# Optimization experiments

Measured on AMD Instinct MI355X. Metric: run time of the kernel, lower is better.

The kernel has to match this reference:

```python
import jax, jax.numpy as jnp
import numpy as np

B, N, F_IN, F_OUT = 8, 2048, 128, 128


def setup_inputs() -> dict:
    key = jax.random.key(0)
    k1, k2, k3, k4 = jax.random.split(key, 4)
    h = jax.random.normal(k1, (B, N, F_IN), dtype=jnp.float32)
    adj = (jax.random.uniform(k2, (B, N, N)) > 0.5).astype(jnp.float32)
    adj = jnp.maximum(adj, jnp.eye(N, dtype=jnp.float32)[None])
    # torch nn.Linear weights: W is [out_features, in_features], a is [1, 2*out_features]
    W = jax.random.normal(k3, (F_OUT, F_IN), dtype=jnp.float32) * 0.05
    a = jax.random.normal(k4, (1, 2 * F_OUT), dtype=jnp.float32) * 0.05
    return {"h": h, "adj": adj, "W": W, "a": a}


def reference(h, adj, W, a):
    # Wh = W(h): [B, N, F_OUT]
    Wh = jnp.einsum("bnf,of->bno", h, W)
    # attn_fc(concat(Wh_i, Wh_j)) == (Wh_i @ a1) + (Wh_j @ a2): exact split of the
    # linear layer, avoiding the O(B*N*N*2F) concat intermediate.
    a1 = a[0, :F_OUT]
    a2 = a[0, F_OUT:]
    e_i = Wh @ a1  # [B, N]  score contribution of destination node i
    e_j = Wh @ a2  # [B, N]  score contribution of source node j
    e = e_i[:, :, None] + e_j[:, None, :]  # [B, N, N]
    e = e + (1.0 - adj) * (-1e9)
    alpha = jax.nn.softmax(e, axis=-1)  # [B, N, N]
    # weighted aggregation: h_out[b,i] = sum_j alpha[b,i,j] * Wh[b,j]
    h_out = jnp.einsum("bij,bjo->bio", alpha, Wh)
    return h_out
```

## Files before the change

kernel.cpp:

```cpp
#include <hip/hip_runtime.h>
#include <stdint.h>

#define AS1 __attribute__((address_space(1)))
#define AS3 __attribute__((address_space(3)))

typedef __bf16 bf16x8 __attribute__((ext_vector_type(8)));
typedef float f32x4 __attribute__((ext_vector_type(4)));

constexpr int NB = 8;
constexpr int N  = 2048;
constexpr int F  = 128;

__device__ __forceinline__ unsigned short bf16r(float f) {
    unsigned u = __float_as_uint(f);
    return (unsigned short)((u + 0x7FFFu + ((u >> 16) & 1u)) >> 16);
}
__device__ __forceinline__ float bf2f(unsigned short s) {
    return __uint_as_float(((unsigned)s) << 16);
}


__global__ __launch_bounds__(256) void k1_wh(const float* __restrict__ h,
                                             const float* __restrict__ W,
                                             const float* __restrict__ a,
                                             unsigned short* __restrict__ Wb2,
                                             unsigned short* __restrict__ p16) {
    __shared__ float epart[2][64];

    const int tid  = threadIdx.x;
    const int lane = tid & 63, wid = tid >> 6;
    const int quad = lane >> 4, l15 = lane & 15;
    const int wm = wid >> 1, wn = wid & 1;
    const int m0 = blockIdx.x * 64;
    const int batch = m0 >> 11;
    const int nbase = m0 & 2047;

    f32x4 acc[2][4] = {};

#pragma unroll
    for (int kk = 0; kk < 4; ++kk) {
        const int k = kk * 32 + quad * 8;
        bf16x8 afr[2], bfr[4];
#pragma unroll
        for (int rt = 0; rt < 2; ++rt) {
            const float* src = h + (size_t)(m0 + wm * 32 + rt * 16 + l15) * F + k;
            float4 x0 = *(const float4*)src;
            float4 x1 = *(const float4*)(src + 4);
            afr[rt][0] = (__bf16)x0.x; afr[rt][1] = (__bf16)x0.y;
            afr[rt][2] = (__bf16)x0.z; afr[rt][3] = (__bf16)x0.w;
            afr[rt][4] = (__bf16)x1.x; afr[rt][5] = (__bf16)x1.y;
            afr[rt][6] = (__bf16)x1.z; afr[rt][7] = (__bf16)x1.w;
        }
#pragma unroll
        for (int ct = 0; ct < 4; ++ct) {
            const int o = wn * 64 + ct * 16 + l15;
            const float* src = W + (size_t)o * F + k;
            float4 x0 = *(const float4*)src;
            float4 x1 = *(const float4*)(src + 4);
            bfr[ct][0] = (__bf16)x0.x; bfr[ct][1] = (__bf16)x0.y;
            bfr[ct][2] = (__bf16)x0.z; bfr[ct][3] = (__bf16)x0.w;
            bfr[ct][4] = (__bf16)x1.x; bfr[ct][5] = (__bf16)x1.y;
            bfr[ct][6] = (__bf16)x1.z; bfr[ct][7] = (__bf16)x1.w;
        }
#pragma unroll
        for (int rt = 0; rt < 2; ++rt)
#pragma unroll
            for (int ct = 0; ct < 4; ++ct)
                acc[rt][ct] = __builtin_amdgcn_mfma_f32_16x16x32_bf16(
                    afr[rt], bfr[ct], acc[rt][ct], 0, 0, 0);
    }

    float a2v[4];
#pragma unroll
    for (int ct = 0; ct < 4; ++ct) a2v[ct] = a[F + wn * 64 + ct * 16 + l15];

    float ep[2][4];
#pragma unroll
    for (int rt = 0; rt < 2; ++rt)
#pragma unroll
        for (int g = 0; g < 4; ++g) {
            float s = 0.f;
#pragma unroll
            for (int ct = 0; ct < 4; ++ct) s += acc[rt][ct][g] * a2v[ct];
            ep[rt][g] = s;
        }
#pragma unroll
    for (int m = 1; m < 16; m <<= 1)
#pragma unroll
        for (int rt = 0; rt < 2; ++rt)
#pragma unroll
            for (int g = 0; g < 4; ++g)
                ep[rt][g] += __shfl_xor(ep[rt][g], m);

    if (l15 == 0)
#pragma unroll
        for (int rt = 0; rt < 2; ++rt)
#pragma unroll
            for (int g = 0; g < 4; ++g)
                epart[wn][wm * 32 + rt * 16 + quad * 4 + g] = ep[rt][g];
    __syncthreads();

#pragma unroll
    for (int rt = 0; rt < 2; ++rt)
#pragma unroll
        for (int ct = 0; ct < 4; ++ct) {
            const int o  = wn * 64 + ct * 16 + l15;
            const int r0 = wm * 32 + rt * 16 + quad * 4;
            const int n0 = nbase + r0;
            ushort4 v;
#pragma unroll
            for (int g = 0; g < 4; ++g) {
                const float e  = epart[0][r0 + g] + epart[1][r0 + g];
                const float pf = bf2f(bf16r(expf(e)));
                (&v.x)[g] = bf16r(pf * acc[rt][ct][g]);
            }
            size_t off = (size_t)batch * N * F + (size_t)(n0 >> 3) * 1024 + o * 8 + (n0 & 7);
            *(ushort4*)&Wb2[off] = v;
        }

    if (tid < 64) {
        const float e = epart[0][tid] + epart[1][tid];
        p16[batch * N + nbase + tid] = bf16r(expf(e));
    }
}

__global__ __launch_bounds__(256) void k3_attn(const float* __restrict__ adj,
                                               const unsigned short* __restrict__ Wb2,
                                               const unsigned short* __restrict__ p16,
                                               float* __restrict__ out) {
    __shared__ __align__(16) float          At[2][32 * 64];
    __shared__ __align__(16) unsigned short Bt[2][8 * 1024];
    __shared__ __align__(16) unsigned short Pt[2048];

    const int tid  = threadIdx.x;
    const int lane = tid & 63, wid = tid >> 6;
    const int quad = lane >> 4, l15 = lane & 15;
    const int wm = wid >> 1, wn = wid & 1;
    const int b  = blockIdx.x & 7;
    const int i0 = (blockIdx.x >> 3) * 32;

    const int lslot = lane & 15;
    const float* aSrcs[2];
#pragma unroll
    for (int s = 0; s < 2; ++s) {
        const int ri = (wid * 2 + s) * 4 + (lane >> 4);
        aSrcs[s] = adj + (size_t)b * N * N + (size_t)(i0 + ri) * N
                 + ((lslot ^ (ri & 15)) << 2);
    }
    const char* bSrc = (const char*)Wb2 + (size_t)b * N * F * 2
                     + (size_t)wid * 4096 + lane * 16;
    const char* pSrc = (const char*)p16 + (size_t)b * N * 2
                     + (size_t)wid * 1024 + lane * 16;

    auto stage = [&](int buf, int c) {
#pragma unroll
        for (int s = 0; s < 2; ++s)
            __builtin_amdgcn_global_load_lds((const AS1 void*)(aSrcs[s] + c * 64),
                (AS3 void*)((char*)&At[buf][0] + (wid * 2 + s) * 1024), 16, 0, 0);
#pragma unroll
        for (int s = 0; s < 4; ++s)
            __builtin_amdgcn_global_load_lds(
                (const AS1 void*)(bSrc + (size_t)c * 16384 + s * 1024),
                (AS3 void*)((char*)&Bt[buf][0] + wid * 4096 + s * 1024), 16, 0, 0);
    };

    f32x4 acc[4] = {};
    f32x4 dacc = {};

    __builtin_amdgcn_global_load_lds((const AS1 void*)pSrc,
        (AS3 void*)((char*)&Pt[0] + wid * 1024), 16, 0, 0);
    stage(0, 0);

    for (int c = 0; c < 32; ++c) {
        const int cur = c & 1;
        __syncthreads();
        if (c + 1 < 32) stage(cur ^ 1, c + 1);

#pragma unroll
        for (int ks = 0; ks < 2; ++ks) {
            const char* rowb = (const char*)&At[cur][0] + (wm * 16 + l15) * 256;
            const int g0 = ks * 8 + quad * 2;
            f32x4 x0 = *(const f32x4*)(rowb + ((g0 ^ l15) << 4));
            f32x4 x1 = *(const f32x4*)(rowb + (((g0 + 1) ^ l15) << 4));
            const char* bb = (const char*)&Bt[cur][0]
                           + (ks * 4 + quad) * 2048 + wn * 1024 + l15 * 16;
            bf16x8 b0 = *(const bf16x8*)bb;
            bf16x8 b1 = *(const bf16x8*)(bb + 256);
            bf16x8 b2 = *(const bf16x8*)(bb + 512);
            bf16x8 b3 = *(const bf16x8*)(bb + 768);
            bf16x8 pv = *(const bf16x8*)((const char*)&Pt[0]
                           + c * 128 + ks * 64 + quad * 16);

            bf16x8 af;
            af[0] = (__bf16)x0[0]; af[1] = (__bf16)x0[1];
            af[2] = (__bf16)x0[2]; af[3] = (__bf16)x0[3];
            af[4] = (__bf16)x1[0]; af[5] = (__bf16)x1[1];
            af[6] = (__bf16)x1[2]; af[7] = (__bf16)x1[3];

            acc[0] = __builtin_amdgcn_mfma_f32_16x16x32_bf16(af, b0, acc[0], 0, 0, 0);
            acc[1] = __builtin_amdgcn_mfma_f32_16x16x32_bf16(af, b1, acc[1], 0, 0, 0);
            acc[2] = __builtin_amdgcn_mfma_f32_16x16x32_bf16(af, b2, acc[2], 0, 0, 0);
            acc[3] = __builtin_amdgcn_mfma_f32_16x16x32_bf16(af, b3, acc[3], 0, 0, 0);
            dacc   = __builtin_amdgcn_mfma_f32_16x16x32_bf16(af, pv, dacc, 0, 0, 0);
        }
    }

    float inv[4];
#pragma unroll
    for (int g = 0; g < 4; ++g) inv[g] = 1.0f / dacc[g];

    float* ob = out + (size_t)b * N * F;
#pragma unroll
    for (int ct = 0; ct < 4; ++ct) {
        const int o = wn * 64 + ct * 16 + l15;
#pragma unroll
        for (int g = 0; g < 4; ++g) {
            const int i = i0 + wm * 16 + quad * 4 + g;
            ob[(size_t)i * F + o] = acc[ct][g] * inv[g];
        }
    }
}

extern "C" void kernel_launch(void* const* d_in, const int* in_sizes, int n_in,
                              void* d_out, int out_size, void* d_ws, size_t ws_size,
                              hipStream_t stream) {
    const float* h   = (const float*)d_in[0];
    const float* adj = (const float*)d_in[1];
    const float* W   = (const float*)d_in[2];
    const float* a   = (const float*)d_in[3];
    float* out = (float*)d_out;

    unsigned short* Wb2 = (unsigned short*)d_ws;
    unsigned short* p16 = (unsigned short*)((char*)d_ws + (4u << 20));

    k1_wh<<<NB * N / 64, 256, 0, stream>>>(h, W, a, Wb2, p16);
    k3_attn<<<NB * (N / 32), 256, 0, stream>>>(adj, Wb2, p16, out);
}
```

Measured before the change: 218.9 us.

## Split attention reduction over source-node quarters with separate reduce kernel

```diff
diff --git a/kernel.cpp b/kernel.cpp
--- a/kernel.cpp
+++ b/kernel.cpp
@@ -10,6 +10,8 @@
 constexpr int NB = 8;
 constexpr int N  = 2048;
 constexpr int F  = 128;
+constexpr size_t NSL = (size_t)NB * N * F;
+constexpr size_t DSL = (size_t)NB * N;
 
 __device__ __forceinline__ unsigned short bf16r(float f) {
     unsigned u = __float_as_uint(f);
@@ -127,98 +129,127 @@
 __global__ __launch_bounds__(256) void k3_attn(const float* __restrict__ adj,
                                                const unsigned short* __restrict__ Wb2,
                                                const unsigned short* __restrict__ p16,
-                                               float* __restrict__ out) {
-    __shared__ __align__(16) float          At[2][32 * 64];
-    __shared__ __align__(16) unsigned short Bt[2][8 * 1024];
-    __shared__ __align__(16) unsigned short Pt[2048];
+                                               float* __restrict__ nump,
+                                               float* __restrict__ denp) {
+    __shared__ __align__(16) float          At[2][64 * 32];
+    __shared__ __align__(16) unsigned short Bt[2][4 * 1024];
+    __shared__ __align__(16) unsigned short Pt[512];
 
     const int tid  = threadIdx.x;
     const int lane = tid & 63, wid = tid >> 6;
     const int quad = lane >> 4, l15 = lane & 15;
     const int wm = wid >> 1, wn = wid & 1;
     const int b  = blockIdx.x & 7;
-    const int i0 = (blockIdx.x >> 3) * 32;
-
-    const int lslot = lane & 15;
+    const int r  = blockIdx.x >> 3;
+    const int it = r >> 2, jq = r & 3;
+    const int i0 = it * 64, j0 = jq * 512;
+
     const float* aSrcs[2];
 #pragma unroll
     for (int s = 0; s < 2; ++s) {
-        const int ri = (wid * 2 + s) * 4 + (lane >> 4);
-        aSrcs[s] = adj + (size_t)b * N * N + (size_t)(i0 + ri) * N
-                 + ((lslot ^ (ri & 15)) << 2);
+        const int ri = (wid * 2 + s) * 8 + (lane >> 3);
+        aSrcs[s] = adj + (size_t)b * N * N + (size_t)(i0 + ri) * N + j0
+                 + (lane & 7) * 4;
     }
     const char* bSrc = (const char*)Wb2 + (size_t)b * N * F * 2
-                     + (size_t)wid * 4096 + lane * 16;
-    const char* pSrc = (const char*)p16 + (size_t)b * N * 2
-                     + (size_t)wid * 1024 + lane * 16;
+                     + (size_t)jq * 131072 + (size_t)wid * 2048 + lane * 16;
+    const char* pSrc = (const char*)p16 + ((size_t)b * N + j0) * 2 + lane * 16;
 
     auto stage = [&](int buf, int c) {
 #pragma unroll
         for (int s = 0; s < 2; ++s)
-            __builtin_amdgcn_global_load_lds((const AS1 void*)(aSrcs[s] + c * 64),
+            __builtin_amdgcn_global_load_lds((const AS1 void*)(aSrcs[s] + c * 32),
                 (AS3 void*)((char*)&At[buf][0] + (wid * 2 + s) * 1024), 16, 0, 0);
 #pragma unroll
-        for (int s = 0; s < 4; ++s)
+        for (int s = 0; s < 2; ++s)
             __builtin_amdgcn_global_load_lds(
-                (const AS1 void*)(bSrc + (size_t)c * 16384 + s * 1024),
-                (AS3 void*)((char*)&Bt[buf][0] + wid * 4096 + s * 1024), 16, 0, 0);
+                (const AS1 void*)(bSrc + (size_t)c * 8192 + s * 1024),
+                (AS3 void*)((char*)&Bt[buf][0] + wid * 2048 + s * 1024), 16, 0, 0);
     };
 
-    f32x4 acc[4] = {};
-    f32x4 dacc = {};
-
-    __builtin_amdgcn_global_load_lds((const AS1 void*)pSrc,
-        (AS3 void*)((char*)&Pt[0] + wid * 1024), 16, 0, 0);
+    f32x4 acc[2][4] = {};
+    f32x4 dacc[2] = {};
+
+    if (wid == 0)
+        __builtin_amdgcn_global_load_lds((const AS1 void*)pSrc,
+            (AS3 void*)((char*)&Pt[0]), 16, 0, 0);
     stage(0, 0);
 
-    for (int c = 0; c < 32; ++c) {
+    for (int c = 0; c < 16; ++c) {
         const int cur = c & 1;
         __syncthreads();
-        if (c + 1 < 32) stage(cur ^ 1, c + 1);
-
-#pragma unroll
-        for (int ks = 0; ks < 2; ++ks) {
-            const char* rowb = (const char*)&At[cur][0] + (wm * 16 + l15) * 256;
-            const int g0 = ks * 8 + quad * 2;
-            f32x4 x0 = *(const f32x4*)(rowb + ((g0 ^ l15) << 4));
-            f32x4 x1 = *(const f32x4*)(rowb + (((g0 + 1) ^ l15) << 4));
+        if (c + 1 < 16) stage(cur ^ 1, c + 1);
+
+        const char* aB = (const char*)&At[cur][0];
+        bf16x8 pv = *(const bf16x8*)((const char*)&Pt[0] + c * 64 + quad * 16);
+
+        bf16x8 af[2];
+#pragma unroll
+        for (int rt = 0; rt < 2; ++rt) {
+            const int row = wm * 32 + rt * 16 + l15;
+            f32x4 x0 = *(const f32x4*)(aB + row * 128 + quad * 32);
+            f32x4 x1 = *(const f32x4*)(aB + row * 128 + quad * 32 + 16);
+            af[rt][0] = (__bf16)x0[0]; af[rt][1] = (__bf16)x0[1];
+            af[rt][2] = (__bf16)x0[2]; af[rt][3] = (__bf16)x0[3];
+            af[rt][4] = (__bf16)x1[0]; af[rt][5] = (__bf16)x1[1];
+            af[rt][6] = (__bf16)x1[2]; af[rt][7] = (__bf16)x1[3];
+        }
+#pragma unroll
+        for (int ct = 0; ct < 4; ++ct) {
             const char* bb = (const char*)&Bt[cur][0]
-                           + (ks * 4 + quad) * 2048 + wn * 1024 + l15 * 16;
-            bf16x8 b0 = *(const bf16x8*)bb;
-            bf16x8 b1 = *(const bf16x8*)(bb + 256);
-            bf16x8 b2 = *(const bf16x8*)(bb + 512);
-            bf16x8 b3 = *(const bf16x8*)(bb + 768);
-            bf16x8 pv = *(const bf16x8*)((const char*)&Pt[0]
-                           + c * 128 + ks * 64 + quad * 16);
-
-            bf16x8 af;
-            af[0] = (__bf16)x0[0]; af[1] = (__bf16)x0[1];
-            af[2] = (__bf16)x0[2]; af[3] = (__bf16)x0[3];
-            af[4] = (__bf16)x1[0]; af[5] = (__bf16)x1[1];
-            af[6] = (__bf16)x1[2]; af[7] = (__bf16)x1[3];
-
-            acc[0] = __builtin_amdgcn_mfma_f32_16x16x32_bf16(af, b0, acc[0], 0, 0, 0);
-            acc[1] = __builtin_amdgcn_mfma_f32_16x16x32_bf16(af, b1, acc[1], 0, 0, 0);
-            acc[2] = __builtin_amdgcn_mfma_f32_16x16x32_bf16(af, b2, acc[2], 0, 0, 0);
-            acc[3] = __builtin_amdgcn_mfma_f32_16x16x32_bf16(af, b3, acc[3], 0, 0, 0);
-            dacc   = __builtin_amdgcn_mfma_f32_16x16x32_bf16(af, pv, dacc, 0, 0, 0);
-        }
-    }
-
-    float inv[4];
-#pragma unroll
-    for (int g = 0; g < 4; ++g) inv[g] = 1.0f / dacc[g];
-
-    float* ob = out + (size_t)b * N * F;
-#pragma unroll
-    for (int ct = 0; ct < 4; ++ct) {
-        const int o = wn * 64 + ct * 16 + l15;
-#pragma unroll
-        for (int g = 0; g < 4; ++g) {
-            const int i = i0 + wm * 16 + quad * 4 + g;
-            ob[(size_t)i * F + o] = acc[ct][g] * inv[g];
-        }
-    }
+                           + quad * 2048 + wn * 1024 + ct * 256 + l15 * 16;
+            bf16x8 bf = *(const bf16x8*)bb;
+#pragma unroll
+            for (int rt = 0; rt < 2; ++rt)
+                acc[rt][ct] = __builtin_amdgcn_mfma_f32_16x16x32_bf16(
+                    af[rt], bf, acc[rt][ct], 0, 0, 0);
+        }
+#pragma unroll
+        for (int rt = 0; rt < 2; ++rt)
+            dacc[rt] = __builtin_amdgcn_mfma_f32_16x16x32_bf16(
+                af[rt], pv, dacc[rt], 0, 0, 0);
+    }
+
+    float* np = nump + (size_t)jq * NSL + (size_t)b * N * F;
+#pragma unroll
+    for (int rt = 0; rt < 2; ++rt)
+#pragma unroll
+        for (int ct = 0; ct < 4; ++ct) {
+            const int o = wn * 64 + ct * 16 + l15;
+#pragma unroll
+            for (int g = 0; g < 4; ++g) {
+                const int i = i0 + wm * 32 + rt * 16 + quad * 4 + g;
+                np[(size_t)i * F + o] = acc[rt][ct][g];
+            }
+        }
+    float* dp = denp + (size_t)jq * DSL + (size_t)b * N;
+#pragma unroll
+    for (int rt = 0; rt < 2; ++rt)
+#pragma unroll
+        for (int g = 0; g < 4; ++g)
+            if (l15 == quad * 4 + g)
+                dp[i0 + wm * 32 + rt * 16 + quad * 4 + g] = dacc[rt][g];
+}
+
+__global__ __launch_bounds__(256) void k4_reduce(const float* __restrict__ nump,
+                                                 const float* __restrict__ denp,
+                                                 float* __restrict__ out) {
+    const int b  = blockIdx.x & 7;
+    const int r0 = (blockIdx.x >> 3) * 8;
+    const int row = r0 + (threadIdx.x >> 5);
+    const int o4  = (threadIdx.x & 31) * 4;
+    const size_t base = ((size_t)b * N + row) * F + o4;
+
+    f32x4 s = {};
+    float d = 0.f;
+#pragma unroll
+    for (int q = 0; q < 4; ++q) {
+        s += *(const f32x4*)&nump[q * NSL + base];
+        d += denp[q * DSL + (size_t)b * N + row];
+    }
+    const float inv = 1.0f / d;
+    f32x4 o = { s[0] * inv, s[1] * inv, s[2] * inv, s[3] * inv };
+    *(f32x4*)&out[base] = o;
 }
 
 extern "C" void kernel_launch(void* const* d_in, const int* in_sizes, int n_in,
@@ -232,7 +263,10 @@
 
     unsigned short* Wb2 = (unsigned short*)d_ws;
     unsigned short* p16 = (unsigned short*)((char*)d_ws + (4u << 20));
+    float* nump = (float*)((char*)d_ws + (8u << 20));
+    float* denp = (float*)((char*)d_ws + (40u << 20));
 
     k1_wh<<<NB * N / 64, 256, 0, stream>>>(h, W, a, Wb2, p16);
-    k3_attn<<<NB * (N / 32), 256, 0, stream>>>(adj, Wb2, p16, out);
-}
+    k3_attn<<<NB * 32 * 4, 256, 0, stream>>>(adj, Wb2, p16, nump, denp);
+    k4_reduce<<<NB * N / 8, 256, 0, stream>>>(nump, denp, out);
+}
```

After: 223.5 us. 1.02x slower.
